# Kernel tuning notes

Hardware: AMD Instinct MI355X
Metric: run time of the kernel (lower is better)

The kernel has to match this reference:

```python
import jax, jax.numpy as jnp
import numpy as np

EPS = 0.3  # residual scaling from init_kwargs
N, E = 50000, 800000
IN_DIM, HID, OUT = 256, 64, 40


def setup_inputs() -> dict:
    key = jax.random.key(0)
    ks = jax.random.split(key, 8)
    h = jax.random.normal(ks[0], (N, IN_DIM), dtype=jnp.float32)
    src = jax.random.randint(ks[1], (E,), 0, N, dtype=jnp.int32)
    dst = jax.random.randint(ks[2], (E,), 0, N, dtype=jnp.int32)
    t1_w = jax.random.normal(ks[3], (HID, IN_DIM), dtype=jnp.float32) * 0.05
    t1_b = jnp.zeros((HID,), jnp.float32)
    gate_w1 = jax.random.normal(ks[4], (2 * HID,), dtype=jnp.float32) * 0.1
    gate_b1 = jnp.zeros((1,), jnp.float32)
    gate_w2 = jax.random.normal(ks[5], (2 * HID,), dtype=jnp.float32) * 0.1
    gate_b2 = jnp.zeros((1,), jnp.float32)
    t2_w = jax.random.normal(ks[6], (OUT, HID), dtype=jnp.float32) * 0.05
    t2_b = jnp.zeros((OUT,), jnp.float32)
    return {"h": h, "src": src, "dst": dst, "t1_w": t1_w, "t1_b": t1_b,
            "gate_w1": gate_w1, "gate_b1": gate_b1,
            "gate_w2": gate_w2, "gate_b2": gate_b2,
            "t2_w": t2_w, "t2_b": t2_b}


def _fa_layer(x, src, dst, d, gate_w, gate_b):
    # gate over concat([h_dst, h_src]) == h_dst @ w[:H] + h_src @ w[H:]
    H = x.shape[1]
    g = jnp.tanh(x[dst] @ gate_w[:H] + x[src] @ gate_w[H:] + gate_b[0])  # [E]
    e = g * d[dst] * d[src]                                              # [E]
    # message: u_mul_e('h','e') then sum onto dst
    z = jnp.zeros_like(x).at[dst].add(x[src] * e[:, None])               # [N,H]
    return z


def reference(h, src, dst, t1_w, t1_b, gate_w1, gate_b1, gate_w2, gate_b2, t2_w, t2_b):
    n = h.shape[0]
    # degree normalization d = deg^{-1/2} (in-degree, clamped to >=1)
    deg = jnp.zeros((n,), h.dtype).at[dst].add(jnp.ones_like(dst, h.dtype))
    d = jax.lax.rsqrt(jnp.maximum(deg, 1.0))
    # dropout is identity in eval mode
    x = jax.nn.relu(h @ t1_w.T + t1_b)
    raw = x
    for gw, gb in ((gate_w1, gate_b1), (gate_w2, gate_b2)):
        x = EPS * raw + _fa_layer(x, src, dst, d, gw, gb)
    logits = x @ t2_w.T + t2_b
    return jax.nn.log_softmax(logits, axis=1)
```

## Files before the change

kernel.cpp:

```cpp
#include <hip/hip_runtime.h>
#include <hip/hip_bf16.h>
#include <math.h>

#define IN_DIM 256
#define HID 64
#define OUT_DIM 40
#define EPS_RES 0.3f
#define NBUK 256
#define CAP 5120
#define EPB 1024

typedef __attribute__((ext_vector_type(8))) short short8v;
typedef __attribute__((ext_vector_type(4))) float f32x4;

__device__ __forceinline__ float tanh_fast(float u) {
    float t = __expf(2.0f * u);
    return 1.0f - 2.0f / (t + 1.0f);
}

__device__ __forceinline__ short f2bf(float f) {
    __hip_bfloat16 b = __float2bfloat16(f);
    return __builtin_bit_cast(short, b);
}

__device__ __forceinline__ float bf2f(unsigned short u) {
    return __builtin_bit_cast(float, (unsigned int)u << 16);
}

__global__ void k_wconv(const float* __restrict__ w1, const float* __restrict__ w2,
                        short* __restrict__ wpre, short* __restrict__ w2p,
                        int* __restrict__ bcur) {
    int i = blockIdx.x * blockDim.x + threadIdx.x;
    if (i < HID * IN_DIM) wpre[i] = f2bf(w1[i]);
    if (i < 48 * HID) {
        int row = i >> 6;
        w2p[i] = f2bf(row < OUT_DIM ? w2[i] : 0.f);
    }
    if (i < NBUK) bcur[i] = 0;
}

__global__ __launch_bounds__(256) void k_bscatter(
    const int* __restrict__ src, const int* __restrict__ dst,
    int* __restrict__ bcur, unsigned int* __restrict__ edges, int E) {
    __shared__ int cnt[NBUK];
    __shared__ int lcur[NBUK];
    int tid = threadIdx.x;
    cnt[tid] = 0;
    __syncthreads();
    int base = blockIdx.x * EPB;
#pragma unroll 4
    for (int k = 0; k < EPB / 256; ++k) {
        int i = base + k * 256 + tid;
        if (i < E) atomicAdd(&cnt[dst[i] >> 8], 1);
    }
    __syncthreads();
    if (cnt[tid]) lcur[tid] = tid * CAP + atomicAdd(&bcur[tid], cnt[tid]);
    __syncthreads();
#pragma unroll 4
    for (int k = 0; k < EPB / 256; ++k) {
        int i = base + k * 256 + tid;
        if (i < E) {
            int d = dst[i];
            int p = atomicAdd(&lcur[d >> 8], 1);
            edges[p] = ((unsigned int)(d & 255) << 16) | (unsigned int)src[i];
        }
    }
}

__global__ __launch_bounds__(256) void k_bfine(
    unsigned int* __restrict__ edges, const int* __restrict__ bcur,
    int* __restrict__ rowp, int* __restrict__ rowe,
    float* __restrict__ dinv, int N) {
    __shared__ unsigned int buf[CAP];
    __shared__ int lc[NBUK];
    __shared__ int sm[NBUK];
    __shared__ int lcur[NBUK];
    int tid = threadIdx.x;
    int b = blockIdx.x;
    int start = b * CAP;
    int cnt = bcur[b];
    lc[tid] = 0;
    __syncthreads();
    for (int k4 = tid * 4; k4 < cnt; k4 += 1024) {
        uint4 v = *(const uint4*)&edges[start + k4];
#pragma unroll
        for (int m = 0; m < 4; ++m) {
            int k = k4 + m;
            if (k < cnt) {
                unsigned int pv = ((const unsigned int*)&v)[m];
                buf[k] = pv;
                atomicAdd(&lc[(pv >> 16) & 255], 1);
            }
        }
    }
    __syncthreads();
    int v = lc[tid];
    sm[tid] = v;
    __syncthreads();
    for (int off = 1; off < NBUK; off <<= 1) {
        int t = (tid >= off) ? sm[tid - off] : 0;
        __syncthreads();
        sm[tid] += t;
        __syncthreads();
    }
    int ls = sm[tid] - v;
    lcur[tid] = ls;
    int node = b * 256 + tid;
    if (node < N) {
        rowp[node] = start + ls;
        rowe[node] = start + ls + v;
        dinv[node] = rsqrtf(fmaxf((float)v, 1.0f));
    }
    __syncthreads();
    for (int k = tid; k < cnt; k += 256) {
        unsigned int pv = buf[k];
        int lo = (pv >> 16) & 255;
        int p = atomicAdd(&lcur[lo], 1);
        edges[start + p] = pv & 0xFFFFu;
    }
}

__global__ __launch_bounds__(256) void k_gemm1(
    const float* __restrict__ h, const short* __restrict__ wpre,
    const float* __restrict__ b, const float* __restrict__ gw,
    const float* __restrict__ dinv,
    short* __restrict__ rawb, short* __restrict__ xsb0,
    float* __restrict__ gpa, float* __restrict__ gpb, int N) {
    int tid = threadIdx.x;
    int lane = tid & 63;
    int l15 = lane & 15, lhi = lane >> 4;
    int wv = __builtin_amdgcn_readfirstlane(tid >> 6);
    int base = blockIdx.x * 128 + wv * 32;

    int ra0 = base + l15;       if (ra0 >= N) ra0 = N - 1;
    int ra1 = base + 16 + l15;  if (ra1 >= N) ra1 = N - 1;
    const float* arow0 = h + (size_t)ra0 * IN_DIM + lhi * 8;
    const float* arow1 = h + (size_t)ra1 * IN_DIM + lhi * 8;

    f32x4 acc0[4] = {{0.f,0.f,0.f,0.f},{0.f,0.f,0.f,0.f},
                     {0.f,0.f,0.f,0.f},{0.f,0.f,0.f,0.f}};
    f32x4 acc1[4] = {{0.f,0.f,0.f,0.f},{0.f,0.f,0.f,0.f},
                     {0.f,0.f,0.f,0.f},{0.f,0.f,0.f,0.f}};

#pragma unroll
    for (int ks = 0; ks < 8; ++ks) {
        const float4* ap0 = (const float4*)(arow0 + ks * 32);
        const float4* ap1 = (const float4*)(arow1 + ks * 32);
        float4 a00 = ap0[0], a01 = ap0[1];
        float4 a10 = ap1[0], a11 = ap1[1];
        short8v af0, af1;
        af0[0] = f2bf(a00.x); af0[1] = f2bf(a00.y);
        af0[2] = f2bf(a00.z); af0[3] = f2bf(a00.w);
        af0[4] = f2bf(a01.x); af0[5] = f2bf(a01.y);
        af0[6] = f2bf(a01.z); af0[7] = f2bf(a01.w);
        af1[0] = f2bf(a10.x); af1[1] = f2bf(a10.y);
        af1[2] = f2bf(a10.z); af1[3] = f2bf(a10.w);
        af1[4] = f2bf(a11.x); af1[5] = f2bf(a11.y);
        af1[6] = f2bf(a11.z); af1[7] = f2bf(a11.w);

        const short* wk = wpre + (size_t)l15 * IN_DIM + ks * 32 + lhi * 8;
#pragma unroll
        for (int t = 0; t < 4; ++t) {
            short8v bf = *(const short8v*)(wk + t * 16 * IN_DIM);
            acc0[t] = __builtin_amdgcn_mfma_f32_16x16x32_bf16(af0, bf, acc0[t], 0, 0, 0);
            acc1[t] = __builtin_amdgcn_mfma_f32_16x16x32_bf16(af1, bf, acc1[t], 0, 0, 0);
        }
    }

#pragma unroll
    for (int half = 0; half < 2; ++half) {
#pragma unroll
        for (int r = 0; r < 4; ++r) {
            int grow = base + half * 16 + lhi * 4 + r;
            float vals[4];
            float pa = 0.f, pb = 0.f;
#pragma unroll
            for (int t = 0; t < 4; ++t) {
                int col = t * 16 + l15;
                float av = half ? acc1[t][r] : acc0[t][r];
                float v = fmaxf(av + b[col], 0.f);
                vals[t] = v;
                pa = fmaf(v, gw[col], pa);
                pb = fmaf(v, gw[HID + col], pb);
            }
            if (grow < N) {
                float dv = dinv[grow];
                short* o  = rawb + (size_t)grow * HID;
                short* os = xsb0 + (size_t)grow * HID;
#pragma unroll
                for (int t = 0; t < 4; ++t) {
                    o[t * 16 + l15]  = f2bf(vals[t]);
                    os[t * 16 + l15] = f2bf(vals[t] * dv);
                }
            }
#pragma unroll
            for (int m = 1; m < 16; m <<= 1) {
                pa += __shfl_xor(pa, m);
                pb += __shfl_xor(pb, m);
            }
            if (l15 == 0 && grow < N) {
                gpa[grow] = pa;
                gpb[grow] = pb;
            }
        }
    }
}

__global__ __launch_bounds__(256) void k_gather(
    const int* __restrict__ rowp, const int* __restrict__ rowe,
    const int* __restrict__ ssrc,
    const float* __restrict__ gpa, const float* __restrict__ gpb,
    const float* __restrict__ dinv, const float* __restrict__ gbias,
    const unsigned short* __restrict__ xsb, const unsigned short* __restrict__ rawb,
    short* __restrict__ zb, int scaled,
    const float* __restrict__ gw_next, float* __restrict__ gpa_next,
    float* __restrict__ gpb_next, int N) {
    int lane = threadIdx.x & 63;
    int wv = __builtin_amdgcn_readfirstlane(threadIdx.x >> 6);
    int t = blockIdx.x * 4 + wv;
    if (t >= N) return;

    float at = gpa[t] + gbias[0];
    float dt = dinv[t];
    float a0v = EPS_RES * bf2f(rawb[((size_t)t << 6) + lane]);
    float a1v = 0.f, a2v = 0.f, a3v = 0.f;
    int k0 = rowp[t];
    int end = rowe[t];

    for (int kc = k0; kc < end; kc += 64) {
        int cnt = end - kc;
        if (cnt > 64) cnt = 64;
        int idx = kc + ((lane < cnt) ? lane : 0);
        int sv = ssrc[idx];
        float ev = tanh_fast(at + gpb[sv]) * dt;
        int evi = __builtin_bit_cast(int, ev);
        int j = 0;
        for (; j + 8 <= cnt; j += 8) {
            int s0 = __builtin_amdgcn_readlane(sv, j);
            int s1 = __builtin_amdgcn_readlane(sv, j + 1);
            int s2 = __builtin_amdgcn_readlane(sv, j + 2);
            int s3 = __builtin_amdgcn_readlane(sv, j + 3);
            int s4 = __builtin_amdgcn_readlane(sv, j + 4);
            int s5 = __builtin_amdgcn_readlane(sv, j + 5);
            int s6 = __builtin_amdgcn_readlane(sv, j + 6);
            int s7 = __builtin_amdgcn_readlane(sv, j + 7);
            float e0 = __builtin_bit_cast(float, __builtin_amdgcn_readlane(evi, j));
            float e1 = __builtin_bit_cast(float, __builtin_amdgcn_readlane(evi, j + 1));
            float e2 = __builtin_bit_cast(float, __builtin_amdgcn_readlane(evi, j + 2));
            float e3 = __builtin_bit_cast(float, __builtin_amdgcn_readlane(evi, j + 3));
            float e4 = __builtin_bit_cast(float, __builtin_amdgcn_readlane(evi, j + 4));
            float e5 = __builtin_bit_cast(float, __builtin_amdgcn_readlane(evi, j + 5));
            float e6 = __builtin_bit_cast(float, __builtin_amdgcn_readlane(evi, j + 6));
            float e7 = __builtin_bit_cast(float, __builtin_amdgcn_readlane(evi, j + 7));
            float x0 = bf2f(xsb[((size_t)s0 << 6) + lane]);
            float x1 = bf2f(xsb[((size_t)s1 << 6) + lane]);
            float x2 = bf2f(xsb[((size_t)s2 << 6) + lane]);
            float x3 = bf2f(xsb[((size_t)s3 << 6) + lane]);
            float x4 = bf2f(xsb[((size_t)s4 << 6) + lane]);
            float x5 = bf2f(xsb[((size_t)s5 << 6) + lane]);
            float x6 = bf2f(xsb[((size_t)s6 << 6) + lane]);
            float x7 = bf2f(xsb[((size_t)s7 << 6) + lane]);
            a0v = fmaf(e0, x0, a0v);
            a1v = fmaf(e1, x1, a1v);
            a2v = fmaf(e2, x2, a2v);
            a3v = fmaf(e3, x3, a3v);
            a0v = fmaf(e4, x4, a0v);
            a1v = fmaf(e5, x5, a1v);
            a2v = fmaf(e6, x6, a2v);
            a3v = fmaf(e7, x7, a3v);
        }
        for (; j + 2 <= cnt; j += 2) {
            int s0 = __builtin_amdgcn_readlane(sv, j);
            int s1 = __builtin_amdgcn_readlane(sv, j + 1);
            float e0 = __builtin_bit_cast(float, __builtin_amdgcn_readlane(evi, j));
            float e1 = __builtin_bit_cast(float, __builtin_amdgcn_readlane(evi, j + 1));
            float x0 = bf2f(xsb[((size_t)s0 << 6) + lane]);
            float x1 = bf2f(xsb[((size_t)s1 << 6) + lane]);
            a0v = fmaf(e0, x0, a0v);
            a1v = fmaf(e1, x1, a1v);
        }
        if (j < cnt) {
            int s0 = __builtin_amdgcn_readlane(sv, j);
            float e0 = __builtin_bit_cast(float, __builtin_amdgcn_readlane(evi, j));
            a0v = fmaf(e0, bf2f(xsb[((size_t)s0 << 6) + lane]), a0v);
        }
    }
    float acc = (a0v + a1v) + (a2v + a3v);
    zb[((size_t)t << 6) + lane] = f2bf(scaled ? dt * acc : acc);

    if (gw_next) {
        float pa = acc * gw_next[lane];
        float pb = acc * gw_next[HID + lane];
#pragma unroll
        for (int m = 32; m; m >>= 1) {
            pa += __shfl_xor(pa, m);
            pb += __shfl_xor(pb, m);
        }
        if (lane == 0) {
            gpa_next[t] = pa;
            gpb_next[t] = pb;
        }
    }
}

__global__ __launch_bounds__(256) void k_head(
    const unsigned short* __restrict__ xb, const short* __restrict__ w2p,
    const float* __restrict__ b2, float* __restrict__ out, int N) {
    int tid = threadIdx.x;
    int lane = tid & 63;
    int l15 = lane & 15, lhi = lane >> 4;
    int wv = __builtin_amdgcn_readfirstlane(tid >> 6);
    int base = blockIdx.x * 128 + wv * 32;

    int ra0 = base + l15;       if (ra0 >= N) ra0 = N - 1;
    int ra1 = base + 16 + l15;  if (ra1 >= N) ra1 = N - 1;
    const short* arow0 = (const short*)(xb + (size_t)ra0 * HID + lhi * 8);
    const short* arow1 = (const short*)(xb + (size_t)ra1 * HID + lhi * 8);

    f32x4 acc0[3] = {{0.f,0.f,0.f,0.f},{0.f,0.f,0.f,0.f},{0.f,0.f,0.f,0.f}};
    f32x4 acc1[3] = {{0.f,0.f,0.f,0.f},{0.f,0.f,0.f,0.f},{0.f,0.f,0.f,0.f}};

#pragma unroll
    for (int ks = 0; ks < 2; ++ks) {
        short8v af0 = *(const short8v*)(arow0 + ks * 32);
        short8v af1 = *(const short8v*)(arow1 + ks * 32);
        const short* wk = w2p + (size_t)l15 * HID + ks * 32 + lhi * 8;
#pragma unroll
        for (int t = 0; t < 3; ++t) {
            short8v bf = *(const short8v*)(wk + t * 16 * HID);
            acc0[t] = __builtin_amdgcn_mfma_f32_16x16x32_bf16(af0, bf, acc0[t], 0, 0, 0);
            acc1[t] = __builtin_amdgcn_mfma_f32_16x16x32_bf16(af1, bf, acc1[t], 0, 0, 0);
        }
    }

    bool has2 = (l15 < 8);
    float b0 = b2[l15];
    float b1 = b2[l15 + 16];
    float bq = has2 ? b2[l15 + 32] : 0.f;

#pragma unroll
    for (int half = 0; half < 2; ++half) {
#pragma unroll
        for (int r = 0; r < 4; ++r) {
            int grow = base + half * 16 + lhi * 4 + r;
            float v0 = (half ? acc1[0][r] : acc0[0][r]) + b0;
            float v1 = (half ? acc1[1][r] : acc0[1][r]) + b1;
            float v2 = (half ? acc1[2][r] : acc0[2][r]) + bq;
            float m = fmaxf(fmaxf(v0, v1), has2 ? v2 : -1e30f);
#pragma unroll
            for (int mm = 1; mm < 16; mm <<= 1) m = fmaxf(m, __shfl_xor(m, mm));
            float s = expf(v0 - m) + expf(v1 - m) + (has2 ? expf(v2 - m) : 0.f);
#pragma unroll
            for (int mm = 1; mm < 16; mm <<= 1) s += __shfl_xor(s, mm);
            float lse = m + logf(s);
            if (grow < N) {
                float* o = out + (size_t)grow * OUT_DIM;
                o[l15] = v0 - lse;
                o[l15 + 16] = v1 - lse;
                if (has2) o[l15 + 32] = v2 - lse;
            }
        }
    }
}

extern "C" void kernel_launch(void* const* d_in, const int* in_sizes, int n_in,
                              void* d_out, int out_size, void* d_ws, size_t ws_size,
                              hipStream_t stream) {
    const float* h    = (const float*)d_in[0];
    const int*   src  = (const int*)d_in[1];
    const int*   dst  = (const int*)d_in[2];
    const float* t1_w = (const float*)d_in[3];
    const float* t1_b = (const float*)d_in[4];
    const float* gw1  = (const float*)d_in[5];
    const float* gb1  = (const float*)d_in[6];
    const float* gw2  = (const float*)d_in[7];
    const float* gb2  = (const float*)d_in[8];
    const float* t2_w = (const float*)d_in[9];
    const float* t2_b = (const float*)d_in[10];
    float* out = (float*)d_out;

    const int N = in_sizes[0] / IN_DIM;
    const int E = in_sizes[1];
    const int NEB = (E + EPB - 1) / EPB;
    const int NBB = (N + 255) / 256;

    short* rawb = (short*)d_ws;
    short* xsb0 = rawb + (size_t)N * HID;
    short* xsb1 = xsb0 + (size_t)N * HID;
    short* xBb  = xsb0;
    float* dinv = (float*)(xsb1 + (size_t)N * HID);
    float* gpa1 = dinv + N;
    float* gpb1 = gpa1 + N;
    float* gpa2 = gpb1 + N;
    float* gpb2 = gpa2 + N;
    short* wpre = (short*)(gpb2 + N);
    short* w2p  = wpre + HID * IN_DIM;
    int* rowp   = (int*)(w2p + 48 * HID);
    int* rowe   = rowp + N;
    int* bcur   = rowe + N;
    unsigned int* edges = (unsigned int*)(bcur + NBUK);

    const int TB = 256;

    k_wconv<<<(HID * IN_DIM + TB - 1) / TB, TB, 0, stream>>>(t1_w, t2_w, wpre, w2p, bcur);

    k_bscatter<<<NEB, TB, 0, stream>>>(src, dst, bcur, edges, E);
    k_bfine<<<NBB, TB, 0, stream>>>(edges, bcur, rowp, rowe, dinv, N);

    k_gemm1<<<(N + 127) / 128, TB, 0, stream>>>(h, wpre, t1_b, gw1, dinv,
                                                rawb, xsb0, gpa1, gpb1, N);

    k_gather<<<(N + 3) / 4, TB, 0, stream>>>(rowp, rowe, (const int*)edges,
                                             gpa1, gpb1, dinv, gb1,
                                             (const unsigned short*)xsb0,
                                             (const unsigned short*)rawb,
                                             xsb1, 1, gw2, gpa2, gpb2, N);

    k_gather<<<(N + 3) / 4, TB, 0, stream>>>(rowp, rowe, (const int*)edges,
                                             gpa2, gpb2, dinv, gb2,
                                             (const unsigned short*)xsb1,
                                             (const unsigned short*)rawb,
                                             xBb, 0, nullptr, nullptr, nullptr, N);

    k_head<<<(N + 127) / 128, TB, 0, stream>>>((const unsigned short*)xBb, w2p, t2_b, out, N);
}
```

Before: 123.7 us.

## Fuse output head and log-softmax into second gather; vectorize bucket scatter loads

The separate head kernel, which ran an MFMA GEMM plus log-softmax, is removed. The second gather layer now computes the 40 logits per node in fp32 through shared memory and does the log-softmax with wave shuffles. This drops a launch, the bf16 round-trip write and read of the final hidden state, and the w2 conversion. In exchange the per-node dot product is scalar FMA work, and lanes 40-63 sit idle. The bucket scatter also reads src and dst as int4 for full blocks, so each thread handles four edges without a loop.

```diff
diff --git a/kernel.cpp b/kernel.cpp
--- a/kernel.cpp
+++ b/kernel.cpp
@@ -27,15 +27,10 @@
     return __builtin_bit_cast(float, (unsigned int)u << 16);
 }
 
-__global__ void k_wconv(const float* __restrict__ w1, const float* __restrict__ w2,
-                        short* __restrict__ wpre, short* __restrict__ w2p,
+__global__ void k_wconv(const float* __restrict__ w1, short* __restrict__ wpre,
                         int* __restrict__ bcur) {
     int i = blockIdx.x * blockDim.x + threadIdx.x;
     if (i < HID * IN_DIM) wpre[i] = f2bf(w1[i]);
-    if (i < 48 * HID) {
-        int row = i >> 6;
-        w2p[i] = f2bf(row < OUT_DIM ? w2[i] : 0.f);
-    }
     if (i < NBUK) bcur[i] = 0;
 }
 
@@ -48,21 +43,42 @@
     cnt[tid] = 0;
     __syncthreads();
     int base = blockIdx.x * EPB;
+    if (base + EPB <= E) {
+        int4 d4 = ((const int4*)(dst + base))[tid];
+        int4 s4 = ((const int4*)(src + base))[tid];
+        atomicAdd(&cnt[d4.x >> 8], 1);
+        atomicAdd(&cnt[d4.y >> 8], 1);
+        atomicAdd(&cnt[d4.z >> 8], 1);
+        atomicAdd(&cnt[d4.w >> 8], 1);
+        __syncthreads();
+        if (cnt[tid]) lcur[tid] = tid * CAP + atomicAdd(&bcur[tid], cnt[tid]);
+        __syncthreads();
+        int p;
+        p = atomicAdd(&lcur[d4.x >> 8], 1);
+        edges[p] = ((unsigned int)(d4.x & 255) << 16) | (unsigned int)s4.x;
+        p = atomicAdd(&lcur[d4.y >> 8], 1);
+        edges[p] = ((unsigned int)(d4.y & 255) << 16) | (unsigned int)s4.y;
+        p = atomicAdd(&lcur[d4.z >> 8], 1);
+        edges[p] = ((unsigned int)(d4.z & 255) << 16) | (unsigned int)s4.z;
+        p = atomicAdd(&lcur[d4.w >> 8], 1);
+        edges[p] = ((unsigned int)(d4.w & 255) << 16) | (unsigned int)s4.w;
+    } else {
 #pragma unroll 4
-    for (int k = 0; k < EPB / 256; ++k) {
-        int i = base + k * 256 + tid;
-        if (i < E) atomicAdd(&cnt[dst[i] >> 8], 1);
-    }
-    __syncthreads();
-    if (cnt[tid]) lcur[tid] = tid * CAP + atomicAdd(&bcur[tid], cnt[tid]);
-    __syncthreads();
+        for (int k = 0; k < EPB / 256; ++k) {
+            int i = base + k * 256 + tid;
+            if (i < E) atomicAdd(&cnt[dst[i] >> 8], 1);
+        }
+        __syncthreads();
+        if (cnt[tid]) lcur[tid] = tid * CAP + atomicAdd(&bcur[tid], cnt[tid]);
+        __syncthreads();
 #pragma unroll 4
-    for (int k = 0; k < EPB / 256; ++k) {
-        int i = base + k * 256 + tid;
-        if (i < E) {
-            int d = dst[i];
-            int p = atomicAdd(&lcur[d >> 8], 1);
-            edges[p] = ((unsigned int)(d & 255) << 16) | (unsigned int)src[i];
+        for (int k = 0; k < EPB / 256; ++k) {
+            int i = base + k * 256 + tid;
+            if (i < E) {
+                int d = dst[i];
+                int p = atomicAdd(&lcur[d >> 8], 1);
+                edges[p] = ((unsigned int)(d & 255) << 16) | (unsigned int)src[i];
+            }
         }
     }
 }
@@ -212,9 +228,12 @@
     const float* __restrict__ gpa, const float* __restrict__ gpb,
     const float* __restrict__ dinv, const float* __restrict__ gbias,
     const unsigned short* __restrict__ xsb, const unsigned short* __restrict__ rawb,
-    short* __restrict__ zb, int scaled,
+    short* __restrict__ zb,
     const float* __restrict__ gw_next, float* __restrict__ gpa_next,
-    float* __restrict__ gpb_next, int N) {
+    float* __restrict__ gpb_next,
+    const float* __restrict__ w2, const float* __restrict__ b2,
+    float* __restrict__ out, int N) {
+    __shared__ float zsm[4][HID];
     int lane = threadIdx.x & 63;
     int wv = __builtin_amdgcn_readfirstlane(threadIdx.x >> 6);
     int t = blockIdx.x * 4 + wv;
@@ -286,7 +305,38 @@
         }
     }
     float acc = (a0v + a1v) + (a2v + a3v);
-    zb[((size_t)t << 6) + lane] = f2bf(scaled ? dt * acc : acc);
+
+    if (out) {
+        zsm[wv][lane] = acc;
+        float logit = 0.f;
+        if (lane < OUT_DIM) {
+            const float4* wr = (const float4*)(w2 + (size_t)lane * HID);
+            const float4* zr = (const float4*)zsm[wv];
+            float lg = b2[lane];
+#pragma unroll
+            for (int q = 0; q < HID / 4; ++q) {
+                float4 w4 = wr[q];
+                float4 z4 = zr[q];
+                lg = fmaf(z4.x, w4.x, lg);
+                lg = fmaf(z4.y, w4.y, lg);
+                lg = fmaf(z4.z, w4.z, lg);
+                lg = fmaf(z4.w, w4.w, lg);
+            }
+            logit = lg;
+        }
+        float mv = (lane < OUT_DIM) ? logit : -1e30f;
+#pragma unroll
+        for (int m = 32; m; m >>= 1) mv = fmaxf(mv, __shfl_xor(mv, m));
+        float ex = (lane < OUT_DIM) ? expf(logit - mv) : 0.f;
+        float sv2 = ex;
+#pragma unroll
+        for (int m = 32; m; m >>= 1) sv2 += __shfl_xor(sv2, m);
+        float lse = mv + logf(sv2);
+        if (lane < OUT_DIM) out[(size_t)t * OUT_DIM + lane] = logit - lse;
+        return;
+    }
+
+    zb[((size_t)t << 6) + lane] = f2bf(dt * acc);
 
     if (gw_next) {
         float pa = acc * gw_next[lane];
@@ -299,66 +349,6 @@
         if (lane == 0) {
             gpa_next[t] = pa;
             gpb_next[t] = pb;
-        }
-    }
-}
-
-__global__ __launch_bounds__(256) void k_head(
-    const unsigned short* __restrict__ xb, const short* __restrict__ w2p,
-    const float* __restrict__ b2, float* __restrict__ out, int N) {
-    int tid = threadIdx.x;
-    int lane = tid & 63;
-    int l15 = lane & 15, lhi = lane >> 4;
-    int wv = __builtin_amdgcn_readfirstlane(tid >> 6);
-    int base = blockIdx.x * 128 + wv * 32;
-
-    int ra0 = base + l15;       if (ra0 >= N) ra0 = N - 1;
-    int ra1 = base + 16 + l15;  if (ra1 >= N) ra1 = N - 1;
-    const short* arow0 = (const short*)(xb + (size_t)ra0 * HID + lhi * 8);
-    const short* arow1 = (const short*)(xb + (size_t)ra1 * HID + lhi * 8);
-
-    f32x4 acc0[3] = {{0.f,0.f,0.f,0.f},{0.f,0.f,0.f,0.f},{0.f,0.f,0.f,0.f}};
-    f32x4 acc1[3] = {{0.f,0.f,0.f,0.f},{0.f,0.f,0.f,0.f},{0.f,0.f,0.f,0.f}};
-
-#pragma unroll
-    for (int ks = 0; ks < 2; ++ks) {
-        short8v af0 = *(const short8v*)(arow0 + ks * 32);
-        short8v af1 = *(const short8v*)(arow1 + ks * 32);
-        const short* wk = w2p + (size_t)l15 * HID + ks * 32 + lhi * 8;
-#pragma unroll
-        for (int t = 0; t < 3; ++t) {
-            short8v bf = *(const short8v*)(wk + t * 16 * HID);
-            acc0[t] = __builtin_amdgcn_mfma_f32_16x16x32_bf16(af0, bf, acc0[t], 0, 0, 0);
-            acc1[t] = __builtin_amdgcn_mfma_f32_16x16x32_bf16(af1, bf, acc1[t], 0, 0, 0);
-        }
-    }
-
-    bool has2 = (l15 < 8);
-    float b0 = b2[l15];
-    float b1 = b2[l15 + 16];
-    float bq = has2 ? b2[l15 + 32] : 0.f;
-
-#pragma unroll
-    for (int half = 0; half < 2; ++half) {
-#pragma unroll
-        for (int r = 0; r < 4; ++r) {
-            int grow = base + half * 16 + lhi * 4 + r;
-            float v0 = (half ? acc1[0][r] : acc0[0][r]) + b0;
-            float v1 = (half ? acc1[1][r] : acc0[1][r]) + b1;
-            float v2 = (half ? acc1[2][r] : acc0[2][r]) + bq;
-            float m = fmaxf(fmaxf(v0, v1), has2 ? v2 : -1e30f);
-#pragma unroll
-            for (int mm = 1; mm < 16; mm <<= 1) m = fmaxf(m, __shfl_xor(m, mm));
-            float s = expf(v0 - m) + expf(v1 - m) + (has2 ? expf(v2 - m) : 0.f);
-#pragma unroll
-            for (int mm = 1; mm < 16; mm <<= 1) s += __shfl_xor(s, mm);
-            float lse = m + logf(s);
-            if (grow < N) {
-                float* o = out + (size_t)grow * OUT_DIM;
-                o[l15] = v0 - lse;
-                o[l15 + 16] = v1 - lse;
-                if (has2) o[l15 + 32] = v2 - lse;
-            }
         }
     }
 }
@@ -387,22 +377,20 @@
     short* rawb = (short*)d_ws;
     short* xsb0 = rawb + (size_t)N * HID;
     short* xsb1 = xsb0 + (size_t)N * HID;
-    short* xBb  = xsb0;
     float* dinv = (float*)(xsb1 + (size_t)N * HID);
     float* gpa1 = dinv + N;
     float* gpb1 = gpa1 + N;
     float* gpa2 = gpb1 + N;
     float* gpb2 = gpa2 + N;
     short* wpre = (short*)(gpb2 + N);
-    short* w2p  = wpre + HID * IN_DIM;
-    int* rowp   = (int*)(w2p + 48 * HID);
+    int* rowp   = (int*)(wpre + HID * IN_DIM);
     int* rowe   = rowp + N;
     int* bcur   = rowe + N;
     unsigned int* edges = (unsigned int*)(bcur + NBUK);
 
     const int TB = 256;
 
-    k_wconv<<<(HID * IN_DIM + TB - 1) / TB, TB, 0, stream>>>(t1_w, t2_w, wpre, w2p, bcur);
+    k_wconv<<<(HID * IN_DIM + TB - 1) / TB, TB, 0, stream>>>(t1_w, wpre, bcur);
 
     k_bscatter<<<NEB, TB, 0, stream>>>(src, dst, bcur, edges, E);
     k_bfine<<<NBB, TB, 0, stream>>>(edges, bcur, rowp, rowe, dinv, N);
@@ -414,13 +402,13 @@
                                              gpa1, gpb1, dinv, gb1,
                                              (const unsigned short*)xsb0,
                                              (const unsigned short*)rawb,
-                                             xsb1, 1, gw2, gpa2, gpb2, N);
+                                             xsb1, gw2, gpa2, gpb2,
+                                             nullptr, nullptr, nullptr, N);
 
     k_gather<<<(N + 3) / 4, TB, 0, stream>>>(rowp, rowe, (const int*)edges,
                                              gpa2, gpb2, dinv, gb2,
                                              (const unsigned short*)xsb1,
                                              (const unsigned short*)rawb,
-                                             xBb, 0, nullptr, nullptr, nullptr, N);
-
-    k_head<<<(N + 127) / 128, TB, 0, stream>>>((const unsigned short*)xBb, w2p, t2_b, out, N);
-}
+                                             nullptr, nullptr, nullptr, nullptr,
+                                             t2_w, t2_b, out, N);
+}
```

After: 164.6 us. 33.1% more time.
